# Performance work log

Hardware: AMD Instinct MI355X
Metric: run time of the kernel (lower is better)

Reference implementation:

```python
import jax, jax.numpy as jnp
import numpy as np

NEG_SLOPE = 0.001

def lrelu(x):
    return jnp.where(x >= 0, x, NEG_SLOPE * x)

def conv1x1(w, x):
    # w: [O, C], x: [B, C, H, W] -> [B, O, H, W]
    return jnp.einsum('oc,bchw->bohw', w, x)

def convk(x, w, pad):
    return jax.lax.conv_general_dilated(
        x, w, window_strides=(1, 1), padding=[(pad, pad), (pad, pad)],
        dimension_numbers=('NCHW', 'OIHW', 'NCHW'))

def setup_inputs() -> dict:
    key = jax.random.key(0)
    ks = jax.random.split(key, 15)
    B, C, H, W = 8, 256, 96, 96
    s = 0.05  # weight scale keeps attention logits well-conditioned
    inp = {
        'x':      jax.random.normal(ks[0], (B, C, H, W), jnp.float32),
        'w_f':    jax.random.normal(ks[1], (16, C), jnp.float32) * s,
        'w_beta': jax.random.normal(ks[2], (C, C), jnp.float32) * s,
        'w1':     jax.random.normal(ks[3], (1, 2, 1, 1), jnp.float32) * s,
        'w3':     jax.random.normal(ks[4], (1, 2, 3, 3), jnp.float32) * s,
        'w5':     jax.random.normal(ks[5], (1, 2, 5, 5), jnp.float32) * s,
        'w7':     jax.random.normal(ks[6], (1, 2, 7, 7), jnp.float32) * s,
        'w_a2b':  jax.random.normal(ks[7], (1, C), jnp.float32) * s,
        'w_f2c':  jax.random.normal(ks[8], (1, 4), jnp.float32) * s,
        'w_f2d':  jax.random.normal(ks[9], (C, 4), jnp.float32) * s,
        'w_e':    jax.random.normal(ks[10], (C, C), jnp.float32) * s,
        'w_h':    jax.random.normal(ks[11], (C, 2 * C), jnp.float32) * s,
        'w_m':    jax.random.normal(ks[12], (C, 2 * C), jnp.float32) * s,
        'w_hm':   jax.random.normal(ks[13], (C, 2 * C), jnp.float32) * s,
    }
    return inp

def reference(x, w_f, w_beta, w1, w3, w5, w7, w_a2b, w_f2c, w_f2d, w_e, w_h, w_m, w_hm):
    B, C, H, W = x.shape
    K = w_f.shape[0]  # output2 = 16

    # ---- ChannelAttention ----
    F = conv1x1(w_f, x).reshape(B, K, H * W)          # [B,16,HW]
    A = x.reshape(B, C, H * W)                        # [B,C,HW]
    S = jax.nn.softmax(jnp.einsum('bkn,bcn->bkc', F, A), axis=2)  # softmax over C
    St = jnp.swapaxes(S, 1, 2)                        # [B,C,16]
    E = jnp.einsum('bck,bkn->bcn', St, F).reshape(B, C, H, W)
    out1 = conv1x1(w_beta, E) + x

    # ---- SpatialAttention ----
    avg_out = jnp.mean(x, axis=1, keepdims=True)
    max_out = jnp.max(x, axis=1, keepdims=True)
    AM = jnp.concatenate([avg_out, max_out], axis=1)  # [B,2,H,W]
    S1 = lrelu(convk(AM, w1, 0))
    S3 = lrelu(convk(AM, w3, 1))
    S5 = lrelu(convk(AM, w5, 2))
    S7 = lrelu(convk(AM, w7, 3))
    Bm = lrelu(conv1x1(w_a2b, x))                     # [B,1,H,W]
    F4 = jnp.concatenate([S1, S3, S5, S7], axis=1)    # [B,4,H,W]
    Cm = lrelu(conv1x1(w_f2c, F4))                    # [B,1,H,W]
    D = lrelu(conv1x1(w_f2d, F4))                     # [B,C,H,W]
    B2 = Bm[:, 0]                                     # [B,H,W]
    # torch: C[idx].view([W, H]) is a row-major reshape, NOT a transpose
    C2 = Cm[:, 0].reshape(B, W, H)                    # [B,W,H]
    Ssp = jax.nn.softmax(jnp.einsum('bhw,bwk->bhk', B2, C2), axis=-1)  # [B,H,H]
    Esp = jnp.einsum('bhk,bckw->bchw', Ssp, D)        # [B,C,H,W]
    out2 = conv1x1(w_e, Esp) + x

    # ---- Fusion ----
    out = jnp.concatenate([out1, out2], axis=1)       # [B,2C,H,W]
    Hh = lrelu(conv1x1(w_h, out))
    M = jax.nn.sigmoid(conv1x1(w_m, jnp.concatenate([Hh, x], axis=1)))
    H_M = lrelu(conv1x1(w_hm, jnp.concatenate([Hh, M], axis=1)))
    return H_M
```

## Files before the change

kernel.cpp:

```cpp
#include <hip/hip_runtime.h>

typedef unsigned short u16;
typedef unsigned int   u32;
typedef unsigned long long u64;

#define BN 8
#define CC 256
#define HW 96
#define NN 9216
#define KK 16

typedef __attribute__((ext_vector_type(8))) short bf16x8;
typedef __attribute__((ext_vector_type(4))) float f32x4;

__device__ __forceinline__ float us2f(u16 u){
  union { u32 i; float f; } v; v.i = ((u32)u) << 16; return v.f;
}
__device__ __forceinline__ u16 f2us(float f){
  union { float f; u32 i; } v; v.f = f;
  u32 x = v.i;
  u32 r = (x + 0x7fffu + ((x >> 16) & 1u)) >> 16;
  return (u16)r;
}
__device__ __forceinline__ float lrelu(float v){ return v >= 0.f ? v : 0.001f*v; }

__device__ __forceinline__ u32 swz7(int n, int c){
  return (u32)(n*512 + ((((c>>3) ^ (n&31)) & 31)<<4) + ((c&7)<<1));
}
__device__ __forceinline__ u32 swz8(int col, int k){
  return (u32)(col*256 + ((((k>>3) ^ (col&15)) & 15)<<4) + ((k&7)<<1));
}

__global__ __launch_bounds__(256) void k1_fx(
    const float* __restrict__ x, const float* __restrict__ w_f, const float* __restrict__ w_a2b,
    float* __restrict__ F, float* __restrict__ AM, float* __restrict__ Bm,
    u16* __restrict__ xf, u16* __restrict__ Ff)
{
  __shared__ float wf[CC][KK];
  __shared__ float wa[CC];
  int t = threadIdx.x;
  for (int i = t; i < KK*CC; i += 256) wf[i & 255][i >> 8] = w_f[i];
  wa[t] = w_a2b[t];
  __syncthreads();
  int pid = blockIdx.x*256 + t;
  int b = pid / NN;
  int n = pid % NN;
  const float* xp = x + (size_t)b*CC*NN + n;
  float a0[KK];
  #pragma unroll
  for (int k=0;k<KK;k++) a0[k]=0.f;
  float s0=0.f, m0=-3e38f, b0=0.f;
  int nt = n >> 4, lnn = n & 15;
  u16* xfb = xf + ((size_t)(b*576 + nt)*8)*512;
  #pragma unroll 2
  for (int c8=0; c8<32; ++c8){
    int cb = c8*8;
    float v[8];
    #pragma unroll
    for (int e=0;e<8;e++) v[e] = xp[(size_t)(cb+e)*NN];
    union { u16 h[8]; uint4 u; } pk;
    #pragma unroll
    for (int e=0;e<8;e++){
      float vv = v[e];
      s0 += vv;
      m0 = fmaxf(m0, vv);
      b0 = fmaf(wa[cb+e], vv, b0);
      const float* wr = wf[cb+e];
      #pragma unroll
      for (int k=0;k<KK;k++) a0[k] = fmaf(wr[k], vv, a0[k]);
      pk.h[e] = f2us(vv);
    }
    int ks = cb >> 5, lkq = (cb >> 3) & 3;
    *reinterpret_cast<uint4*>(xfb + ((size_t)ks*64 + lkq*16 + lnn)*8) = pk.u;
  }
  float* Fp = F + (size_t)b*KK*NN + n;
  #pragma unroll
  for (int k=0;k<KK;k++) Fp[(size_t)k*NN] = a0[k];
  u16* ffb = Ff + (size_t)(b*576 + nt)*512;
  union { u16 h[8]; uint4 u; } pk2;
  #pragma unroll
  for (int lkq=0; lkq<2; lkq++){
    #pragma unroll
    for (int e=0;e<8;e++) pk2.h[e] = f2us(a0[lkq*8+e]);
    *reinterpret_cast<uint4*>(ffb + ((size_t)lkq*16 + lnn)*8) = pk2.u;
  }
  uint4 z; z.x=z.y=z.z=z.w=0u;
  *reinterpret_cast<uint4*>(ffb + ((size_t)2*16 + lnn)*8) = z;
  *reinterpret_cast<uint4*>(ffb + ((size_t)3*16 + lnn)*8) = z;
  AM[(size_t)b*2*NN + n] = s0*(1.f/256.f);
  AM[(size_t)b*2*NN + NN + n] = m0;
  Bm[(size_t)b*NN + n] = lrelu(b0);
}

__global__ __launch_bounds__(256) void k2_g(
    const float* __restrict__ x, const float* __restrict__ F, float* __restrict__ G)
{
  int b = blockIdx.x >> 6;
  int c0 = (blockIdx.x & 63) * 4;
  int t = threadIdx.x;
  const float* Fp = F + (size_t)b*KK*NN;
  const float* xp = x + ((size_t)b*CC + c0)*NN;
  float acc[KK][4];
  #pragma unroll
  for (int k=0;k<KK;k++){ acc[k][0]=acc[k][1]=acc[k][2]=acc[k][3]=0.f; }
  for (int n = t; n < NN; n += 256){
    float xv0 = xp[n];
    float xv1 = xp[(size_t)NN + n];
    float xv2 = xp[(size_t)2*NN + n];
    float xv3 = xp[(size_t)3*NN + n];
    #pragma unroll
    for (int k=0;k<KK;k++){
      float fv = Fp[(size_t)k*NN + n];
      acc[k][0] = fmaf(fv, xv0, acc[k][0]);
      acc[k][1] = fmaf(fv, xv1, acc[k][1]);
      acc[k][2] = fmaf(fv, xv2, acc[k][2]);
      acc[k][3] = fmaf(fv, xv3, acc[k][3]);
    }
  }
  #pragma unroll
  for (int k=0;k<KK;k++){
    #pragma unroll
    for (int i=0;i<4;i++){
      float v = acc[k][i];
      for (int off=32; off>0; off>>=1) v += __shfl_down(v, off);
      acc[k][i] = v;
    }
  }
  __shared__ float part[4][KK][4];
  int lane = t & 63, wv = t >> 6;
  if (lane == 0){
    #pragma unroll
    for (int k=0;k<KK;k++){ part[wv][k][0]=acc[k][0]; part[wv][k][1]=acc[k][1];
                            part[wv][k][2]=acc[k][2]; part[wv][k][3]=acc[k][3]; }
  }
  __syncthreads();
  if (t < 64){
    int k = t >> 2, i = t & 3;
    float s = part[0][k][i] + part[1][k][i] + part[2][k][i] + part[3][k][i];
    G[((size_t)b*KK + k)*CC + c0 + i] = s;
  }
}

__global__ __launch_bounds__(256) void k3_smws(
    const float* __restrict__ G, const float* __restrict__ w_beta, u16* __restrict__ wspk)
{
  int b = blockIdx.x, t = threadIdx.x;
  __shared__ float sl[KK][CC];
  for (int k=0;k<KK;k++) sl[k][t] = G[((size_t)b*KK + k)*CC + t];
  __syncthreads();
  int lane = t & 63, wv = t >> 6;
  for (int r=0;r<4;r++){
    int k = wv*4 + r;
    float v0 = sl[k][lane], v1 = sl[k][lane+64], v2 = sl[k][lane+128], v3 = sl[k][lane+192];
    float m = fmaxf(fmaxf(v0,v1), fmaxf(v2,v3));
    for (int off=32; off>0; off>>=1) m = fmaxf(m, __shfl_xor(m, off));
    float e0=__expf(v0-m), e1=__expf(v1-m), e2=__expf(v2-m), e3=__expf(v3-m);
    float s = e0+e1+e2+e3;
    for (int off=32; off>0; off>>=1) s += __shfl_xor(s, off);
    float inv = 1.f/s;
    sl[k][lane]=e0*inv; sl[k][lane+64]=e1*inv; sl[k][lane+128]=e2*inv; sl[k][lane+192]=e3*inv;
  }
  __syncthreads();
  const float* wb = w_beta + (size_t)t*CC;
  float acc[KK];
  #pragma unroll
  for (int k=0;k<KK;k++) acc[k]=0.f;
  for (int c=0;c<CC;c++){
    float w = wb[c];
    #pragma unroll
    for (int k=0;k<KK;k++) acc[k] = fmaf(w, sl[k][c], acc[k]);
  }
  int ot = t >> 4, lo = t & 15;
  union { u16 h[8]; uint4 u; } pk;
  #pragma unroll
  for (int lkq=0; lkq<2; lkq++){
    #pragma unroll
    for (int e=0;e<8;e++) pk.h[e] = f2us(acc[lkq*8+e]);
    *reinterpret_cast<uint4*>(wspk + ((size_t)(b*16 + ot)*64 + lkq*16 + lo)*8) = pk.u;
  }
  uint4 z; z.x=z.y=z.z=z.w=0u;
  *reinterpret_cast<uint4*>(wspk + ((size_t)(b*16 + ot)*64 + 2*16 + lo)*8) = z;
  *reinterpret_cast<uint4*>(wspk + ((size_t)(b*16 + ot)*64 + 3*16 + lo)*8) = z;
}

__global__ __launch_bounds__(256) void k5_conv(
    const float* __restrict__ AM, const float* __restrict__ w1, const float* __restrict__ w3,
    const float* __restrict__ w5, const float* __restrict__ w7, const float* __restrict__ wf2c,
    float* __restrict__ F4, float* __restrict__ Cm)
{
  __shared__ float w3l[18], w5l[50], w7l[98], w1l[2], wcl[4];
  int t = threadIdx.x;
  if (t < 2)  w1l[t] = w1[t];
  if (t < 18) w3l[t] = w3[t];
  if (t < 50) w5l[t] = w5[t];
  if (t < 98) w7l[t] = w7[t];
  if (t < 4)  wcl[t] = wf2c[t];
  __syncthreads();
  int gid = blockIdx.x*256 + t;
  int b = gid / NN, n = gid % NN;
  int h = n / HW, w = n % HW;
  const float* am = AM + (size_t)b*2*NN;
  float a0 = am[n], a1 = am[NN + n];
  float s1v = lrelu(a0*w1l[0] + a1*w1l[1]);
  float s3v=0.f, s5v=0.f, s7v=0.f;
  for (int p=-3;p<=3;p++){
    int hh = h + p;
    if (hh < 0 || hh >= HW) continue;
    for (int q=-3;q<=3;q++){
      int ww = w + q;
      if (ww < 0 || ww >= HW) continue;
      float v0 = am[hh*HW+ww], v1 = am[NN + hh*HW + ww];
      s7v += v0*w7l[(p+3)*7 + (q+3)] + v1*w7l[49 + (p+3)*7 + (q+3)];
      if (p>=-2 && p<=2 && q>=-2 && q<=2)
        s5v += v0*w5l[(p+2)*5 + (q+2)] + v1*w5l[25 + (p+2)*5 + (q+2)];
      if (p>=-1 && p<=1 && q>=-1 && q<=1)
        s3v += v0*w3l[(p+1)*3 + (q+1)] + v1*w3l[9 + (p+1)*3 + (q+1)];
    }
  }
  s3v = lrelu(s3v); s5v = lrelu(s5v); s7v = lrelu(s7v);
  float* f4p = F4 + (size_t)b*4*NN + n;
  f4p[0] = s1v; f4p[NN] = s3v; f4p[2*(size_t)NN] = s5v; f4p[3*(size_t)NN] = s7v;
  Cm[(size_t)b*NN + n] = lrelu(s1v*wcl[0] + s3v*wcl[1] + s5v*wcl[2] + s7v*wcl[3]);
}

__global__ __launch_bounds__(256) void k6a_t(
    const float* __restrict__ Bm, const float* __restrict__ Cm, float* __restrict__ Tsc)
{
  __shared__ float Cl[NN];
  int b = blockIdx.x, t = threadIdx.x;
  for (int i=t;i<NN;i+=256) Cl[i] = Cm[(size_t)b*NN + i];
  __syncthreads();
  const float* bp = Bm + (size_t)b*NN;
  for (int g=0; g<9; g++){
    int idx4 = (t + 256*g)*4;
    int h = idx4/96, k0 = idx4%96;
    float a0=0.f,a1=0.f,a2=0.f,a3=0.f;
    const float* brow = bp + h*96;
    for (int w2=0;w2<96;w2++){
      float bv = brow[w2];
      float4 cv = *reinterpret_cast<const float4*>(&Cl[w2*96 + k0]);
      a0=fmaf(bv,cv.x,a0); a1=fmaf(bv,cv.y,a1); a2=fmaf(bv,cv.z,a2); a3=fmaf(bv,cv.w,a3);
    }
    float4 o4; o4.x=a0; o4.y=a1; o4.z=a2; o4.w=a3;
    *reinterpret_cast<float4*>(Tsc + (size_t)b*NN + idx4) = o4;
  }
}

__global__ __launch_bounds__(256) void k6b_sm(
    const float* __restrict__ Tsc, u16* __restrict__ spk)
{
  int gid = blockIdx.x*256 + threadIdx.x;
  if (gid >= BN*96) return;
  int b = gid/96, h = gid%96;
  const float* row = Tsc + (size_t)b*NN + h*96;
  float m = -3e38f;
  for (int k=0;k<96;k++) m = fmaxf(m, row[k]);
  float s = 0.f;
  for (int k=0;k<96;k++) s += __expf(row[k]-m);
  float inv = 1.f/s;
  int mf = h >> 4;
  for (int g=0; g<12; g++){
    int ks = g >> 2, lk = g & 3;
    union { u16 hh[8]; uint4 u; } pk;
    #pragma unroll
    for (int e=0;e<8;e++) pk.hh[e] = f2us(__expf(row[g*8+e]-m)*inv);
    *reinterpret_cast<uint4*>(spk + ((size_t)(((b*6 + mf)*3 + ks)*64) + lk*16 + (h&15))*8) = pk.u;
  }
}

__global__ __launch_bounds__(256) void kw_pack(
    const float* __restrict__ w_h, const float* __restrict__ w_m,
    const float* __restrict__ w_hm, const float* __restrict__ w_e,
    u16* __restrict__ wpk, u16* __restrict__ wpkE)
{
  int gid = blockIdx.x*256 + threadIdx.x;
  if (gid < 49152){
    int mat = gid >> 14;
    int r = gid & 16383;
    int ot = r >> 10;
    int ks = (r >> 6) & 15;
    int l  = r & 63;
    const float* W = (mat==0) ? w_h : ((mat==1) ? w_m : w_hm);
    int o = ot*16 + (l & 15);
    int c = ks*32 + (l >> 4)*8;
    const float* src = W + (size_t)o*512 + c;
    union { u16 h[8]; uint4 u; } pk;
    #pragma unroll
    for (int e=0;e<8;e++) pk.h[e] = f2us(src[e]);
    *reinterpret_cast<uint4*>(wpk + (size_t)gid*8) = pk.u;
  } else {
    int r = gid - 49152;
    int ot = r >> 9;
    int ks = (r >> 6) & 7;
    int l  = r & 63;
    int o = ot*16 + (l & 15);
    int c = ks*32 + (l >> 4)*8;
    const float* src = w_e + (size_t)o*256 + c;
    union { u16 h[8]; uint4 u; } pk;
    #pragma unroll
    for (int e=0;e<8;e++) pk.h[e] = f2us(src[e]);
    *reinterpret_cast<uint4*>(wpkE + (size_t)r*8) = pk.u;
  }
}

__global__ __launch_bounds__(256) void k7m(
    const float* __restrict__ F4, const float* __restrict__ w_f2d,
    const u16* __restrict__ wpkE, u16* __restrict__ WD)
{
  __shared__ uint4 sm4[2048];
  char* sm = reinterpret_cast<char*>(sm4);
  int t = threadIdx.x;
  int b = blockIdx.x / 144;
  int n0 = (blockIdx.x % 144) * 64;
  int n = t & 63, cg = t >> 6;
  float f0 = F4[((size_t)b*4+0)*NN + n0 + n];
  float f1 = F4[((size_t)b*4+1)*NN + n0 + n];
  float f2 = F4[((size_t)b*4+2)*NN + n0 + n];
  float f3 = F4[((size_t)b*4+3)*NN + n0 + n];
  for (int c8 = 0; c8 < 8; ++c8){
    int c = cg*64 + c8*8;
    union { u16 h[8]; uint4 u; } pk;
    #pragma unroll
    for (int e=0;e<8;e++){
      const float* wfp = w_f2d + (size_t)(c+e)*4;
      pk.h[e] = f2us(lrelu(fmaf(wfp[0],f0, fmaf(wfp[1],f1, fmaf(wfp[2],f2, wfp[3]*f3)))));
    }
    *reinterpret_cast<uint4*>(sm + swz7(n, c)) = pk.u;
  }
  __syncthreads();
  int w = t >> 6, l = t & 63, ln = l & 15, lk = l >> 4;
  f32x4 acc[4][4];
  #pragma unroll
  for (int i=0;i<4;i++){ acc[i][0]=0.f; acc[i][1]=0.f; acc[i][2]=0.f; acc[i][3]=0.f; }
  for (int ks=0; ks<8; ++ks){
    bf16x8 bfr[4];
    #pragma unroll
    for (int nf=0; nf<4; nf++)
      bfr[nf] = *reinterpret_cast<const bf16x8*>(sm + swz7(nf*16 + ln, ks*32 + lk*8));
    #pragma unroll
    for (int mf=0; mf<4; mf++){
      bf16x8 afr = *reinterpret_cast<const bf16x8*>(wpkE + ((size_t)((w*4+mf)*8 + ks)*64 + l)*8);
      #pragma unroll
      for (int nf=0; nf<4; nf++)
        acc[mf][nf] = __builtin_amdgcn_mfma_f32_16x16x32_bf16(afr, bfr[nf], acc[mf][nf], 0,0,0);
    }
  }
  #pragma unroll
  for (int mf=0; mf<4; mf++){
    #pragma unroll
    for (int nf=0; nf<4; nf++){
      #pragma unroll
      for (int r=0;r<4;r++){
        int o = (w*4+mf)*16 + lk*4 + r;
        WD[((size_t)b*CC + o)*NN + n0 + nf*16 + ln] = f2us(acc[mf][nf][r]);
      }
    }
  }
}

__global__ __launch_bounds__(256) void k8m(
    const u16* __restrict__ WD, const u16* __restrict__ spk, u16* __restrict__ P)
{
  __shared__ uint4 sm4[3072];
  char* sm = reinterpret_cast<char*>(sm4);
  int t = threadIdx.x;
  int b = blockIdx.x >> 7;
  int o0 = (blockIdx.x & 127) * 2;
  for (int it=0; it<9; ++it){
    int s = it*256 + t;
    int w16 = s % 12;
    int k   = (s / 12) % 96;
    int oi  = s / 1152;
    union { u16 h[8]; uint4 u; } v;
    v.u = *reinterpret_cast<const uint4*>(WD + ((size_t)b*CC + o0+oi)*NN + k*96 + w16*8);
    #pragma unroll
    for (int e=0;e<8;e++){
      int col = oi*96 + w16*8 + e;
      *reinterpret_cast<u16*>(sm + swz8(col, k)) = v.h[e];
    }
  }
  __syncthreads();
  int w = t >> 6, l = t & 63, ln = l & 15, lk = l >> 4;
  f32x4 acc[6][3];
  #pragma unroll
  for (int i=0;i<6;i++){ acc[i][0]=0.f; acc[i][1]=0.f; acc[i][2]=0.f; }
  for (int ks=0; ks<3; ++ks){
    bf16x8 bfr[3];
    #pragma unroll
    for (int j=0;j<3;j++){
      int col = (w*3 + j)*16 + ln;
      bfr[j] = *reinterpret_cast<const bf16x8*>(sm + swz8(col, ks*32 + lk*8));
    }
    #pragma unroll
    for (int mf=0; mf<6; mf++){
      bf16x8 afr = *reinterpret_cast<const bf16x8*>(spk + ((size_t)(((b*6 + mf)*3 + ks)*64) + l)*8);
      #pragma unroll
      for (int j=0;j<3;j++)
        acc[mf][j] = __builtin_amdgcn_mfma_f32_16x16x32_bf16(afr, bfr[j], acc[mf][j], 0,0,0);
    }
  }
  #pragma unroll
  for (int j=0;j<3;j++){
    int col = (w*3 + j)*16 + ln;
    int oi = (col >= 96) ? 1 : 0;
    int ww = col - 96*oi;
    u16* op = P + ((size_t)b*CC + o0+oi)*NN + ww;
    #pragma unroll
    for (int mf=0; mf<6; mf++){
      #pragma unroll
      for (int r=0;r<4;r++){
        int h = mf*16 + lk*4 + r;
        op[(size_t)h*96] = f2us(acc[mf][j][r]);
      }
    }
  }
}

#define TP 72
__global__ __launch_bounds__(256) void k8t(
    const u16* __restrict__ P, const u16* __restrict__ xf, u16* __restrict__ o2t)
{
  __shared__ u16 tl[256*TP];
  int t = threadIdx.x;
  int b = blockIdx.x / 144;
  int tile = blockIdx.x % 144;
  int n0 = tile * 64;
  for (int it=0; it<8; ++it){
    int o = it*32 + (t >> 3);
    int nb = t & 7;
    uint4 v = *reinterpret_cast<const uint4*>(P + ((size_t)b*CC + o)*NN + n0 + nb*8);
    *reinterpret_cast<uint4*>(&tl[o*TP + nb*8]) = v;
  }
  __syncthreads();
  for (int it=0; it<8; ++it){
    int g = it*256 + t;
    int nt_loc = g >> 9;
    int ks = (g >> 6) & 7;
    int lane = g & 63;
    int lkq = lane >> 4, lnn = lane & 15;
    int ob = ks*32 + lkq*8;
    int n_loc = nt_loc*16 + lnn;
    union { u16 h[8]; uint4 u; } gr;
    #pragma unroll
    for (int e=0;e<8;e++) gr.h[e] = tl[(ob+e)*TP + n_loc];
    size_t fo = (((size_t)(b*576 + tile*4 + nt_loc)*8 + ks)*64 + lkq*16 + lnn)*8;
    uint4 xv = *reinterpret_cast<const uint4*>(xf + fo);
    const u32* xp2 = reinterpret_cast<const u32*>(&xv);
    union { u16 h[8]; uint4 u; } res;
    #pragma unroll
    for (int q=0;q<4;q++){
      u32 xw = xp2[q];
      res.h[2*q+0] = f2us(us2f(gr.h[2*q+0]) + us2f((u16)(xw & 0xffffu)));
      res.h[2*q+1] = f2us(us2f(gr.h[2*q+1]) + us2f((u16)(xw >> 16)));
    }
    *reinterpret_cast<uint4*>(o2t + fo) = res.u;
  }
}

__global__ __launch_bounds__(512) void k910(
    const u16* __restrict__ o2t, const u16* __restrict__ xf,
    const u16* __restrict__ Ff, const u16* __restrict__ wspk,
    const u16* __restrict__ wpkH, const u16* __restrict__ wpkM,
    const u16* __restrict__ wpkHM, float* __restrict__ out)
{
  __shared__ uint4 sm4[4096];
  char* sm = reinterpret_cast<char*>(sm4);
  int t = threadIdx.x;
  int b = blockIdx.x / 144;
  int tile = blockIdx.x % 144;
  int n0 = tile * 64;
  int w = t >> 6, l = t & 63, ln = l & 15, lk = l >> 4;
  {
    bf16x8 fb[4];
    #pragma unroll
    for (int nf=0; nf<4; nf++)
      fb[nf] = *reinterpret_cast<const bf16x8*>(Ff + (size_t)(b*576 + tile*4 + nf)*512 + (size_t)l*8);
    #pragma unroll
    for (int mf=0; mf<2; mf++){
      bf16x8 afr = *reinterpret_cast<const bf16x8*>(wspk + ((size_t)(b*16 + w*2 + mf)*64 + l)*8);
      int obase = w*32 + mf*16 + lk*4;
      #pragma unroll
      for (int nf=0; nf<4; nf++){
        f32x4 zz = {0.f,0.f,0.f,0.f};
        f32x4 a1 = __builtin_amdgcn_mfma_f32_16x16x32_bf16(afr, fb[nf], zz, 0,0,0);
        int n = nf*16 + ln;
        int nt = tile*4 + nf;
        u64 xv4 = *reinterpret_cast<const u64*>(
            xf + (((size_t)(b*576 + nt)*8 + (obase>>5))*64 + ((obase>>3)&3)*16 + ln)*8 + (obase&7));
        union { u16 h[4]; u64 u; } pk;
        #pragma unroll
        for (int r=0;r<4;r++)
          pk.h[r] = f2us(a1[r] + us2f((u16)(xv4 >> (16*r))));
        *reinterpret_cast<u64*>(sm + 32768 + swz7(n, obase)) = pk.u;
      }
    }
  }
  __syncthreads();
  f32x4 acc[2][4];
  #pragma unroll
  for (int i=0;i<2;i++){ acc[i][0]=0.f; acc[i][1]=0.f; acc[i][2]=0.f; acc[i][3]=0.f; }
  #pragma unroll 2
  for (int ks=0; ks<16; ++ks){
    bf16x8 bfr[4];
    if (ks < 8){
      int c = ks*32 + lk*8;
      #pragma unroll
      for (int nf=0; nf<4; nf++)
        bfr[nf] = *reinterpret_cast<const bf16x8*>(sm + 32768 + swz7(nf*16 + ln, c));
    } else {
      #pragma unroll
      for (int nf=0; nf<4; nf++)
        bfr[nf] = *reinterpret_cast<const bf16x8*>(o2t + (((size_t)(b*576 + tile*4 + nf)*8 + (ks-8))*64 + l)*8);
    }
    #pragma unroll
    for (int mf=0; mf<2; mf++){
      bf16x8 afr = *reinterpret_cast<const bf16x8*>(wpkH + ((size_t)((w*2+mf)*16 + ks)*64 + l)*8);
      #pragma unroll
      for (int nf=0; nf<4; nf++)
        acc[mf][nf] = __builtin_amdgcn_mfma_f32_16x16x32_bf16(afr, bfr[nf], acc[mf][nf], 0,0,0);
    }
  }
  __syncthreads();
  #pragma unroll
  for (int mf=0; mf<2; mf++){
    int obase = w*32 + mf*16 + lk*4;
    #pragma unroll
    for (int nf=0; nf<4; nf++){
      int n = nf*16 + ln;
      union { u16 h[4]; u64 u; } pk;
      #pragma unroll
      for (int r=0;r<4;r++) pk.h[r] = f2us(lrelu(acc[mf][nf][r]));
      *reinterpret_cast<u64*>(sm + 32768 + swz7(n, obase)) = pk.u;
    }
  }
  __syncthreads();
  #pragma unroll
  for (int i=0;i<2;i++){ acc[i][0]=0.f; acc[i][1]=0.f; acc[i][2]=0.f; acc[i][3]=0.f; }
  #pragma unroll 2
  for (int ks=0; ks<16; ++ks){
    bf16x8 bfr[4];
    if (ks < 8){
      int c = ks*32 + lk*8;
      #pragma unroll
      for (int nf=0; nf<4; nf++)
        bfr[nf] = *reinterpret_cast<const bf16x8*>(sm + 32768 + swz7(nf*16 + ln, c));
    } else {
      #pragma unroll
      for (int nf=0; nf<4; nf++)
        bfr[nf] = *reinterpret_cast<const bf16x8*>(xf + (((size_t)(b*576 + tile*4 + nf)*8 + (ks-8))*64 + l)*8);
    }
    #pragma unroll
    for (int mf=0; mf<2; mf++){
      bf16x8 afr = *reinterpret_cast<const bf16x8*>(wpkM + ((size_t)((w*2+mf)*16 + ks)*64 + l)*8);
      #pragma unroll
      for (int nf=0; nf<4; nf++)
        acc[mf][nf] = __builtin_amdgcn_mfma_f32_16x16x32_bf16(afr, bfr[nf], acc[mf][nf], 0,0,0);
    }
  }
  #pragma unroll
  for (int mf=0; mf<2; mf++){
    int obase = w*32 + mf*16 + lk*4;
    #pragma unroll
    for (int nf=0; nf<4; nf++){
      int n = nf*16 + ln;
      union { u16 h[4]; u64 u; } pk;
      #pragma unroll
      for (int r=0;r<4;r++) pk.h[r] = f2us(1.f/(1.f + __expf(-acc[mf][nf][r])));
      *reinterpret_cast<u64*>(sm + swz7(n, obase)) = pk.u;
    }
  }
  __syncthreads();
  #pragma unroll
  for (int i=0;i<2;i++){ acc[i][0]=0.f; acc[i][1]=0.f; acc[i][2]=0.f; acc[i][3]=0.f; }
  #pragma unroll 2
  for (int ks=0; ks<16; ++ks){
    int c = (ks & 7)*32 + lk*8;
    int roff = (ks < 8) ? 32768 : 0;
    bf16x8 bfr[4];
    #pragma unroll
    for (int nf=0; nf<4; nf++)
      bfr[nf] = *reinterpret_cast<const bf16x8*>(sm + roff + swz7(nf*16 + ln, c));
    #pragma unroll
    for (int mf=0; mf<2; mf++){
      bf16x8 afr = *reinterpret_cast<const bf16x8*>(wpkHM + ((size_t)((w*2+mf)*16 + ks)*64 + l)*8);
      #pragma unroll
      for (int nf=0; nf<4; nf++)
        acc[mf][nf] = __builtin_amdgcn_mfma_f32_16x16x32_bf16(afr, bfr[nf], acc[mf][nf], 0,0,0);
    }
  }
  #pragma unroll
  for (int mf=0; mf<2; mf++){
    #pragma unroll
    for (int nf=0; nf<4; nf++){
      #pragma unroll
      for (int r=0;r<4;r++){
        int o = w*32 + mf*16 + lk*4 + r;
        out[((size_t)b*CC + o)*NN + n0 + nf*16 + ln] = lrelu(acc[mf][nf][r]);
      }
    }
  }
}

extern "C" void kernel_launch(void* const* d_in, const int* in_sizes, int n_in,
                              void* d_out, int out_size, void* d_ws, size_t ws_size,
                              hipStream_t stream)
{
  const float* x     = (const float*)d_in[0];
  const float* w_f   = (const float*)d_in[1];
  const float* w_beta= (const float*)d_in[2];
  const float* w1    = (const float*)d_in[3];
  const float* w3    = (const float*)d_in[4];
  const float* w5    = (const float*)d_in[5];
  const float* w7    = (const float*)d_in[6];
  const float* w_a2b = (const float*)d_in[7];
  const float* w_f2c = (const float*)d_in[8];
  const float* w_f2d = (const float*)d_in[9];
  const float* w_e   = (const float*)d_in[10];
  const float* w_h   = (const float*)d_in[11];
  const float* w_m   = (const float*)d_in[12];
  const float* w_hm  = (const float*)d_in[13];

  char* ws = (char*)d_ws;
  size_t off = 0;
  auto alloc = [&](size_t bytes) -> void* {
    void* p = ws + off; off += (bytes + 255) & ~(size_t)255; return p;
  };
  float* F    = (float*)alloc(sizeof(float)*(size_t)BN*KK*NN);
  float* AMb  = (float*)alloc(sizeof(float)*(size_t)BN*2*NN);
  float* Bmv  = (float*)alloc(sizeof(float)*(size_t)BN*NN);
  float* Cmv  = (float*)alloc(sizeof(float)*(size_t)BN*NN);
  float* F4   = (float*)alloc(sizeof(float)*(size_t)BN*4*NN);
  float* G    = (float*)alloc(sizeof(float)*(size_t)BN*KK*CC);
  float* Tsc  = (float*)alloc(sizeof(float)*(size_t)BN*NN);
  u16*   spk  = (u16*)alloc(sizeof(u16)*(size_t)BN*NN);
  u16*   WD   = (u16*)alloc(sizeof(u16)*(size_t)BN*CC*NN);
  u16*   Pm   = (u16*)alloc(sizeof(u16)*(size_t)BN*CC*NN);
  u16*   o2t  = (u16*)alloc(sizeof(u16)*(size_t)BN*CC*NN);
  u16*   xf   = (u16*)alloc(sizeof(u16)*(size_t)BN*CC*NN);
  u16*   Ff   = (u16*)alloc(sizeof(u16)*(size_t)BN*576*512);
  u16*   wpk  = (u16*)alloc(sizeof(u16)*(size_t)3*16384*8);
  u16*   wpkE = (u16*)alloc(sizeof(u16)*(size_t)8192*8);
  u16*   wspk = (u16*)alloc(sizeof(u16)*(size_t)BN*16*64*8);
  (void)ws_size; (void)in_sizes; (void)n_in; (void)out_size;

  u16* wpkH  = wpk;
  u16* wpkM  = wpk + (size_t)16384*8;
  u16* wpkHM = wpk + (size_t)2*16384*8;

  kw_pack <<<224, 256, 0, stream>>>(w_h, w_m, w_hm, w_e, wpk, wpkE);
  k1_fx   <<<288, 256, 0, stream>>>(x, w_f, w_a2b, F, AMb, Bmv, xf, Ff);
  k2_g    <<<512, 256, 0, stream>>>(x, F, G);
  k3_smws <<<8,   256, 0, stream>>>(G, w_beta, wspk);
  k5_conv <<<288, 256, 0, stream>>>(AMb, w1, w3, w5, w7, w_f2c, F4, Cmv);
  k6a_t   <<<8,   256, 0, stream>>>(Bmv, Cmv, Tsc);
  k6b_sm  <<<3,   256, 0, stream>>>(Tsc, spk);
  k7m     <<<1152,256, 0, stream>>>(F4, w_f2d, wpkE, WD);
  k8m     <<<1024,256, 0, stream>>>(WD, spk, Pm);
  k8t     <<<1152,256, 0, stream>>>(Pm, xf, o2t);
  k910    <<<1152,512, 0, stream>>>(o2t, xf, Ff, wspk, wpkH, wpkM, wpkHM, (float*)d_out);
}
```

Baseline: 328.8 us.

## Split k1 channel loop across two half-blocks and fuse spatial logits with softmax

k1_fx now runs 512 threads per block, with each half reducing 128 channels. Partial sums are combined through shared memory, which doubles the memory-level parallelism for the x read. The spatial logits GEMM and its softmax are merged into one kernel launched on 64 blocks (per batch, 12 rows each) instead of 8 plus 3 blocks. This removes the Tsc global round trip and one launch, and spreads the serial logits work over more CUs. The cost is extra shared memory, a sync, and each block reloading the full Cm slice.

```diff
diff --git a/kernel.cpp b/kernel.cpp
--- a/kernel.cpp
+++ b/kernel.cpp
@@ -31,18 +31,21 @@
   return (u32)(col*256 + ((((k>>3) ^ (col&15)) & 15)<<4) + ((k&7)<<1));
 }
 
-__global__ __launch_bounds__(256) void k1_fx(
+__global__ __launch_bounds__(512) void k1_fx(
     const float* __restrict__ x, const float* __restrict__ w_f, const float* __restrict__ w_a2b,
     float* __restrict__ F, float* __restrict__ AM, float* __restrict__ Bm,
     u16* __restrict__ xf, u16* __restrict__ Ff)
 {
   __shared__ float wf[CC][KK];
   __shared__ float wa[CC];
-  int t = threadIdx.x;
-  for (int i = t; i < KK*CC; i += 256) wf[i & 255][i >> 8] = w_f[i];
-  wa[t] = w_a2b[t];
-  __syncthreads();
-  int pid = blockIdx.x*256 + t;
+  __shared__ float pa[256][KK];
+  __shared__ float ps[256], pm[256], pb[256];
+  int t = threadIdx.x;
+  for (int i = t; i < KK*CC; i += 512) wf[i & 255][i >> 8] = w_f[i];
+  if (t < CC) wa[t] = w_a2b[t];
+  __syncthreads();
+  int half = t >> 8, tp = t & 255;
+  int pid = blockIdx.x*256 + tp;
   int b = pid / NN;
   int n = pid % NN;
   const float* xp = x + (size_t)b*CC*NN + n;
@@ -52,9 +55,10 @@
   float s0=0.f, m0=-3e38f, b0=0.f;
   int nt = n >> 4, lnn = n & 15;
   u16* xfb = xf + ((size_t)(b*576 + nt)*8)*512;
+  int cb0 = half*128;
   #pragma unroll 2
-  for (int c8=0; c8<32; ++c8){
-    int cb = c8*8;
+  for (int c8=0; c8<16; ++c8){
+    int cb = cb0 + c8*8;
     float v[8];
     #pragma unroll
     for (int e=0;e<8;e++) v[e] = xp[(size_t)(cb+e)*NN];
@@ -73,23 +77,34 @@
     int ks = cb >> 5, lkq = (cb >> 3) & 3;
     *reinterpret_cast<uint4*>(xfb + ((size_t)ks*64 + lkq*16 + lnn)*8) = pk.u;
   }
-  float* Fp = F + (size_t)b*KK*NN + n;
-  #pragma unroll
-  for (int k=0;k<KK;k++) Fp[(size_t)k*NN] = a0[k];
-  u16* ffb = Ff + (size_t)(b*576 + nt)*512;
-  union { u16 h[8]; uint4 u; } pk2;
-  #pragma unroll
-  for (int lkq=0; lkq<2; lkq++){
-    #pragma unroll
-    for (int e=0;e<8;e++) pk2.h[e] = f2us(a0[lkq*8+e]);
-    *reinterpret_cast<uint4*>(ffb + ((size_t)lkq*16 + lnn)*8) = pk2.u;
-  }
-  uint4 z; z.x=z.y=z.z=z.w=0u;
-  *reinterpret_cast<uint4*>(ffb + ((size_t)2*16 + lnn)*8) = z;
-  *reinterpret_cast<uint4*>(ffb + ((size_t)3*16 + lnn)*8) = z;
-  AM[(size_t)b*2*NN + n] = s0*(1.f/256.f);
-  AM[(size_t)b*2*NN + NN + n] = m0;
-  Bm[(size_t)b*NN + n] = lrelu(b0);
+  if (half){
+    #pragma unroll
+    for (int k=0;k<KK;k++) pa[tp][k] = a0[k];
+    ps[tp] = s0; pm[tp] = m0; pb[tp] = b0;
+  }
+  __syncthreads();
+  if (!half){
+    #pragma unroll
+    for (int k=0;k<KK;k++) a0[k] += pa[tp][k];
+    s0 += ps[tp]; m0 = fmaxf(m0, pm[tp]); b0 += pb[tp];
+    float* Fp = F + (size_t)b*KK*NN + n;
+    #pragma unroll
+    for (int k=0;k<KK;k++) Fp[(size_t)k*NN] = a0[k];
+    u16* ffb = Ff + (size_t)(b*576 + nt)*512;
+    union { u16 h[8]; uint4 u; } pk2;
+    #pragma unroll
+    for (int lkq=0; lkq<2; lkq++){
+      #pragma unroll
+      for (int e=0;e<8;e++) pk2.h[e] = f2us(a0[lkq*8+e]);
+      *reinterpret_cast<uint4*>(ffb + ((size_t)lkq*16 + lnn)*8) = pk2.u;
+    }
+    uint4 z; z.x=z.y=z.z=z.w=0u;
+    *reinterpret_cast<uint4*>(ffb + ((size_t)2*16 + lnn)*8) = z;
+    *reinterpret_cast<uint4*>(ffb + ((size_t)3*16 + lnn)*8) = z;
+    AM[(size_t)b*2*NN + n] = s0*(1.f/256.f);
+    AM[(size_t)b*2*NN + NN + n] = m0;
+    Bm[(size_t)b*NN + n] = lrelu(b0);
+  }
 }
 
 __global__ __launch_bounds__(256) void k2_g(
@@ -223,48 +238,48 @@
   Cm[(size_t)b*NN + n] = lrelu(s1v*wcl[0] + s3v*wcl[1] + s5v*wcl[2] + s7v*wcl[3]);
 }
 
-__global__ __launch_bounds__(256) void k6a_t(
-    const float* __restrict__ Bm, const float* __restrict__ Cm, float* __restrict__ Tsc)
+__global__ __launch_bounds__(256) void k6ab(
+    const float* __restrict__ Bm, const float* __restrict__ Cm, u16* __restrict__ spk)
 {
   __shared__ float Cl[NN];
-  int b = blockIdx.x, t = threadIdx.x;
-  for (int i=t;i<NN;i+=256) Cl[i] = Cm[(size_t)b*NN + i];
-  __syncthreads();
-  const float* bp = Bm + (size_t)b*NN;
-  for (int g=0; g<9; g++){
-    int idx4 = (t + 256*g)*4;
-    int h = idx4/96, k0 = idx4%96;
-    float a0=0.f,a1=0.f,a2=0.f,a3=0.f;
-    const float* brow = bp + h*96;
-    for (int w2=0;w2<96;w2++){
-      float bv = brow[w2];
-      float4 cv = *reinterpret_cast<const float4*>(&Cl[w2*96 + k0]);
-      a0=fmaf(bv,cv.x,a0); a1=fmaf(bv,cv.y,a1); a2=fmaf(bv,cv.z,a2); a3=fmaf(bv,cv.w,a3);
-    }
-    float4 o4; o4.x=a0; o4.y=a1; o4.z=a2; o4.w=a3;
-    *reinterpret_cast<float4*>(Tsc + (size_t)b*NN + idx4) = o4;
-  }
-}
-
-__global__ __launch_bounds__(256) void k6b_sm(
-    const float* __restrict__ Tsc, u16* __restrict__ spk)
-{
-  int gid = blockIdx.x*256 + threadIdx.x;
-  if (gid >= BN*96) return;
-  int b = gid/96, h = gid%96;
-  const float* row = Tsc + (size_t)b*NN + h*96;
-  float m = -3e38f;
-  for (int k=0;k<96;k++) m = fmaxf(m, row[k]);
-  float s = 0.f;
-  for (int k=0;k<96;k++) s += __expf(row[k]-m);
-  float inv = 1.f/s;
-  int mf = h >> 4;
-  for (int g=0; g<12; g++){
-    int ks = g >> 2, lk = g & 3;
-    union { u16 hh[8]; uint4 u; } pk;
-    #pragma unroll
-    for (int e=0;e<8;e++) pk.hh[e] = f2us(__expf(row[g*8+e]-m)*inv);
-    *reinterpret_cast<uint4*>(spk + ((size_t)(((b*6 + mf)*3 + ks)*64) + lk*16 + (h&15))*8) = pk.u;
+  __shared__ float Tl[12][96];
+  int t = threadIdx.x;
+  int b = blockIdx.x >> 3;
+  int hg = blockIdx.x & 7;
+  for (int i=t; i<NN/4; i+=256)
+    *reinterpret_cast<float4*>(&Cl[i*4]) = *reinterpret_cast<const float4*>(&Cm[(size_t)b*NN + i*4]);
+  __syncthreads();
+  const float* bp = Bm + (size_t)b*NN + (size_t)hg*12*96;
+  for (int g=0; g<2; ++g){
+    int idx = g*256 + t;
+    if (idx < 288){
+      int hr = idx/24, k0 = (idx%24)*4;
+      const float* brow = bp + hr*96;
+      float a0=0.f,a1=0.f,a2=0.f,a3=0.f;
+      for (int w2=0; w2<96; ++w2){
+        float bv = brow[w2];
+        float4 cv = *reinterpret_cast<const float4*>(&Cl[w2*96 + k0]);
+        a0=fmaf(bv,cv.x,a0); a1=fmaf(bv,cv.y,a1); a2=fmaf(bv,cv.z,a2); a3=fmaf(bv,cv.w,a3);
+      }
+      Tl[hr][k0]=a0; Tl[hr][k0+1]=a1; Tl[hr][k0+2]=a2; Tl[hr][k0+3]=a3;
+    }
+  }
+  __syncthreads();
+  if (t < 12){
+    int h = hg*12 + t;
+    float m = -3e38f;
+    for (int k=0;k<96;k++) m = fmaxf(m, Tl[t][k]);
+    float s = 0.f;
+    for (int k=0;k<96;k++) s += __expf(Tl[t][k]-m);
+    float inv = 1.f/s;
+    int mf = h >> 4;
+    for (int g=0; g<12; g++){
+      int ks = g >> 2, lk = g & 3;
+      union { u16 hh[8]; uint4 u; } pk;
+      #pragma unroll
+      for (int e=0;e<8;e++) pk.hh[e] = f2us(__expf(Tl[t][g*8+e]-m)*inv);
+      *reinterpret_cast<uint4*>(spk + ((size_t)(((b*6 + mf)*3 + ks)*64) + lk*16 + (h&15))*8) = pk.u;
+    }
   }
 }
 
@@ -631,7 +646,6 @@
   float* Cmv  = (float*)alloc(sizeof(float)*(size_t)BN*NN);
   float* F4   = (float*)alloc(sizeof(float)*(size_t)BN*4*NN);
   float* G    = (float*)alloc(sizeof(float)*(size_t)BN*KK*CC);
-  float* Tsc  = (float*)alloc(sizeof(float)*(size_t)BN*NN);
   u16*   spk  = (u16*)alloc(sizeof(u16)*(size_t)BN*NN);
   u16*   WD   = (u16*)alloc(sizeof(u16)*(size_t)BN*CC*NN);
   u16*   Pm   = (u16*)alloc(sizeof(u16)*(size_t)BN*CC*NN);
@@ -648,12 +662,11 @@
   u16* wpkHM = wpk + (size_t)2*16384*8;
 
   kw_pack <<<224, 256, 0, stream>>>(w_h, w_m, w_hm, w_e, wpk, wpkE);
-  k1_fx   <<<288, 256, 0, stream>>>(x, w_f, w_a2b, F, AMb, Bmv, xf, Ff);
+  k1_fx   <<<288, 512, 0, stream>>>(x, w_f, w_a2b, F, AMb, Bmv, xf, Ff);
   k2_g    <<<512, 256, 0, stream>>>(x, F, G);
   k3_smws <<<8,   256, 0, stream>>>(G, w_beta, wspk);
   k5_conv <<<288, 256, 0, stream>>>(AMb, w1, w3, w5, w7, w_f2c, F4, Cmv);
-  k6a_t   <<<8,   256, 0, stream>>>(Bmv, Cmv, Tsc);
-  k6b_sm  <<<3,   256, 0, stream>>>(Tsc, spk);
+  k6ab    <<<64,  256, 0, stream>>>(Bmv, Cmv, spk);
   k7m     <<<1152,256, 0, stream>>>(F4, w_f2d, wpkE, WD);
   k8m     <<<1024,256, 0, stream>>>(WD, spk, Pm);
   k8t     <<<1152,256, 0, stream>>>(Pm, xf, o2t);
```

New measurement: 281.7 us. -14.3%, faster.
